# Kernel tuning notes

Measured on AMD Instinct MI355X. Metric: run time of the kernel, lower is better.

Reference implementation:

```python
import jax, jax.numpy as jnp
import numpy as np

DIM = 256
NUM_HEADS = 4
HEAD_DIM = DIM // NUM_HEADS
SCALE = HEAD_DIM ** -0.5
LN_EPS = 1e-5


def setup_inputs() -> dict:
    key = jax.random.key(0)
    ks = jax.random.split(key, 12)
    V, B, C, H, W = 3, 2, DIM, 32, 32
    s = 0.02
    return {
        "features": jax.random.normal(ks[0], (V, B, C, H, W), jnp.float32),
        "Wq": jax.random.normal(ks[1], (DIM, DIM), jnp.float32) * s,
        "bq": jnp.zeros((DIM,), jnp.float32),
        "Wk": jax.random.normal(ks[2], (DIM, DIM), jnp.float32) * s,
        "bk": jnp.zeros((DIM,), jnp.float32),
        "Wv": jax.random.normal(ks[3], (DIM, DIM), jnp.float32) * s,
        "bv": jnp.zeros((DIM,), jnp.float32),
        "Wp": jax.random.normal(ks[4], (DIM, DIM), jnp.float32) * s,
        "bp": jnp.zeros((DIM,), jnp.float32),
        "gamma": jnp.ones((DIM,), jnp.float32),
        "beta": jnp.zeros((DIM,), jnp.float32),
    }


def reference(features, Wq, bq, Wk, bk, Wv, bv, Wp, bp, gamma, beta):
    V, B, C, H, W = features.shape
    N = H * W
    L = V * N
    # concat views along token axis: [B, V*N, C]
    x = features.reshape(V, B, C, N).transpose(1, 0, 3, 2).reshape(B, L, C)
    # QKV projections (torch Linear: x @ W.T + b)
    q = (x @ Wq.T + bq).reshape(B, L, NUM_HEADS, HEAD_DIM).transpose(0, 2, 1, 3)
    k = (x @ Wk.T + bk).reshape(B, L, NUM_HEADS, HEAD_DIM).transpose(0, 2, 1, 3)
    v = (x @ Wv.T + bv).reshape(B, L, NUM_HEADS, HEAD_DIM).transpose(0, 2, 1, 3)
    # full attention (chunked loop in original is exact, dropout off in eval)
    attn = jax.nn.softmax(jnp.einsum('bhqd,bhkd->bhqk', q, k) * SCALE, axis=-1)
    o = jnp.einsum('bhqk,bhkd->bhqd', attn, v)  # [B, H, L, D]
    o = o.transpose(0, 2, 1, 3).reshape(B, L, C)
    # output proj + LayerNorm
    o = o @ Wp.T + bp
    mu = jnp.mean(o, axis=-1, keepdims=True)
    var = jnp.mean(jnp.square(o - mu), axis=-1, keepdims=True)
    o = (o - mu) * jax.lax.rsqrt(var + LN_EPS) * gamma + beta
    # mean over views, back to [B, C, H, W]
    o = o.reshape(B, V, N, C).mean(axis=1)
    return o.reshape(B, H, W, C).transpose(0, 3, 1, 2)
```

## Files before the change

### kernel.cpp

```cpp
#include <hip/hip_runtime.h>
#include <hip/hip_bf16.h>

#define V_ 3
#define B_ 2
#define C_ 256
#define N_ 1024
#define L_ 3072
#define NH 4
#define DH 64
#define SCALE 0.125f
#define LOG2E 1.44269504088896340736f

typedef __attribute__((ext_vector_type(8))) short short8;
typedef __attribute__((ext_vector_type(4))) float floatx4;
typedef unsigned short u16;
typedef unsigned int u32;

__device__ __forceinline__ u16 f2bf(float f) {
    union { float f; u32 u; } c; c.f = f;
    u32 u = c.u;
    u32 lsb = (u >> 16) & 1u;
    u += 0x7fffu + lsb;
    return (u16)(u >> 16);
}
__device__ __forceinline__ u32 pk_bf16(float a, float b) {
    __hip_bfloat162 h = __float22bfloat162_rn(make_float2(a, b));
    union { __hip_bfloat162 h; u32 u; } cv; cv.h = h; return cv.u;
}

__global__ __launch_bounds__(256) void k_prep_gather(
    const float* __restrict__ feat,
    const float* __restrict__ Wq, const float* __restrict__ Wk,
    const float* __restrict__ Wv, const float* __restrict__ Wp,
    u16* __restrict__ x, u16* __restrict__ Wb) {
    int bid = blockIdx.x;
    int t = threadIdx.x;
    if (bid < 384) {
        __shared__ u16 tile[64][66];
        int n0 = (bid & 15) << 6;
        int c0 = ((bid >> 4) & 3) << 6;
        int b  = (bid >> 6) & 1;
        int v  = bid >> 7;
        const float* src = feat + ((size_t)((v * B_ + b) * C_ + c0)) * N_ + n0;
        for (int i = 0; i < 8; ++i) {
            int idx = i * 256 + t;
            int cl = idx >> 5;
            int np2 = idx & 31;
            float2 f = *(const float2*)(src + (size_t)cl * N_ + np2 * 2);
            *(u32*)&tile[cl][np2 * 2] = pk_bf16(f.x, f.y);
        }
        __syncthreads();
        u16* dst = x + ((size_t)(b * L_ + v * N_ + n0)) * C_ + c0;
        for (int i = 0; i < 8; ++i) {
            int idx = i * 256 + t;
            int nl = idx >> 5;
            int cl = (idx & 31) * 2;
            u32 uu = (u32)tile[cl][nl] | ((u32)tile[cl + 1][nl] << 16);
            *(u32*)(dst + (size_t)nl * C_ + cl) = uu;
        }
    } else {
        int idx = (bid - 384) * 256 + t;
        int g0 = idx * 16;
        int m = g0 >> 16;
        const float* src = (m == 0) ? Wq : (m == 1) ? Wk : (m == 2) ? Wv : Wp;
        int off = g0 & 65535;
#pragma unroll
        for (int e = 0; e < 8; ++e) {
            float2 f = *(const float2*)(src + off + e * 2);
            ((u32*)(Wb + g0))[e] = pk_bf16(f.x, f.y);
        }
    }
}


__global__ __launch_bounds__(64) void k_qkv(
    const u16* __restrict__ x, const u16* __restrict__ Wb,
    const float* __restrict__ bq, const float* __restrict__ bk,
    const float* __restrict__ bv,
    u16* __restrict__ Qf, u16* __restrict__ Kf, u16* __restrict__ Vf) {
    int bid = blockIdx.x;
    int npc = bid & 3;
    int rest = bid >> 2;
    int m  = rest / 192;
    int rb = rest % 192;
    int b  = rb / 96;
    int r0 = (rb % 96) * 32;
    int lane = threadIdx.x;
    int quad = lane >> 4, m16 = lane & 15;

    const u16* xrow0 = x + ((size_t)(b * L_ + r0 + m16)) * C_ + quad * 8;
    const u16* xrow1 = xrow0 + (size_t)16 * C_;
    short8 a0[8], a1[8];
#pragma unroll
    for (int kc = 0; kc < 8; ++kc) {
        a0[kc] = *(const short8*)(xrow0 + kc * 32);
        a1[kc] = *(const short8*)(xrow1 + kc * 32);
    }

    const u16* W   = Wb + (size_t)m * 65536;
    const float* bs = (m == 0) ? bq : (m == 1) ? bk : bv;
    float scale = (m == 0) ? (SCALE * LOG2E) : 1.0f;

#pragma unroll
    for (int np = npc * 2; np < npc * 2 + 2; ++np) {
        int nt0 = np * 2;
        const u16* w0 = W + (size_t)(nt0 * 16 + m16) * C_ + quad * 8;
        const u16* w1 = w0 + 16 * C_;
        short8 wf0[8], wf1[8];
#pragma unroll
        for (int kc = 0; kc < 8; ++kc) {
            wf0[kc] = *(const short8*)(w0 + kc * 32);
            wf1[kc] = *(const short8*)(w1 + kc * 32);
        }
        floatx4 acc00 = {0.f,0.f,0.f,0.f}, acc01 = {0.f,0.f,0.f,0.f};
        floatx4 acc10 = {0.f,0.f,0.f,0.f}, acc11 = {0.f,0.f,0.f,0.f};
#pragma unroll
        for (int kc = 0; kc < 8; ++kc) {
            acc00 = __builtin_amdgcn_mfma_f32_16x16x32_bf16(a0[kc], wf0[kc], acc00, 0, 0, 0);
            acc01 = __builtin_amdgcn_mfma_f32_16x16x32_bf16(a0[kc], wf1[kc], acc01, 0, 0, 0);
            acc10 = __builtin_amdgcn_mfma_f32_16x16x32_bf16(a1[kc], wf0[kc], acc10, 0, 0, 0);
            acc11 = __builtin_amdgcn_mfma_f32_16x16x32_bf16(a1[kc], wf1[kc], acc11, 0, 0, 0);
        }
#pragma unroll
        for (int gi = 0; gi < 2; ++gi)
#pragma unroll
        for (int half = 0; half < 2; ++half) {
            int dout = (nt0 + half) * 16 + m16;
            float bias = bs[dout];
            int h = dout >> 6, dh = dout & 63;
            size_t bh = (size_t)(b * NH + h);
            floatx4 acc = gi ? (half ? acc11 : acc10) : (half ? acc01 : acc00);
            float f0 = (acc[0] + bias) * scale, f1 = (acc[1] + bias) * scale;
            float f2 = (acc[2] + bias) * scale, f3 = (acc[3] + bias) * scale;
            int lr0 = r0 + gi * 16 + quad * 4;
            if (m == 2) {
                int tile = lr0 >> 6, kk = lr0 & 63;
                int halfv = kk >> 5, quadp = (kk >> 3) & 3, j0 = kk & 7;
                int ntv = dh >> 4, m16pp = dh & 15;
                u32* p = (u32*)(Vf + (bh * 48 + tile) * 4096 +
                                ((size_t)((ntv * 2 + halfv) * 64 + quadp * 16 + m16pp)) * 8 + j0);
                p[0] = pk_bf16(f0, f1);
                p[1] = pk_bf16(f2, f3);
            } else {
                int cc = dh >> 5, quadp = (dh >> 3) & 3, j = dh & 7;
                u32 p01 = pk_bf16(f0, f1);
                u32 p23 = pk_bf16(f2, f3);
                if (m == 0) {
#pragma unroll
                    for (int r = 0; r < 4; ++r) {
                        int lr = lr0 + r;
                        int grp = lr >> 4, m16p = lr & 15;
                        u32 pk = (r < 2) ? p01 : p23;
                        u16 val = (r & 1) ? (u16)(pk >> 16) : (u16)pk;
                        Qf[(bh * 192 + grp) * 1024 +
                           (size_t)(cc * 64 + quadp * 16 + m16p) * 8 + j] = val;
                    }
                } else {
#pragma unroll
                    for (int r = 0; r < 4; ++r) {
                        int lr = lr0 + r;
                        int tile = lr >> 6, rr = lr & 63;
                        int ntk = rr >> 4, m16p = rr & 15;
                        u32 pk = (r < 2) ? p01 : p23;
                        u16 val = (r & 1) ? (u16)(pk >> 16) : (u16)pk;
                        Kf[(bh * 48 + tile) * 4096 +
                           (size_t)((ntk * 2 + cc) * 64 + quadp * 16 + m16p) * 8 + j] = val;
                    }
                }
            }
        }
    }
}

__global__ __launch_bounds__(256, 3) void k_attn(
    const u16* __restrict__ Qf, const u16* __restrict__ Kf,
    const u16* __restrict__ Vf, u16* __restrict__ o) {
    __shared__ __align__(16) u16 p_lds[4][32][72];
    __shared__ float o_red[3][32][65];
    __shared__ float l_red[3][32];
    int bid = blockIdx.x;
    int qt = bid % 96;
    int h  = (bid / 96) & 3;
    int b  = bid / 384;
    int lane = threadIdx.x & 63;
    int w    = threadIdx.x >> 6;
    int quad = lane >> 4, m16 = lane & 15;
    int q0 = qt * 32;
    size_t bh = (size_t)(b * NH + h);

    const u16* qbase = Qf + (bh * 192 + qt * 2) * 1024 + (size_t)lane * 8;
    const u16* kbase = Kf + bh * 48 * 4096 + (size_t)lane * 8;
    const u16* vbase = Vf + bh * 48 * 4096 + (size_t)lane * 8;

    short8 aq[2][2];
    aq[0][0] = *(const short8*)(qbase);
    aq[0][1] = *(const short8*)(qbase + 512);
    aq[1][0] = *(const short8*)(qbase + 1024);
    aq[1][1] = *(const short8*)(qbase + 1536);

    float l_s[2][4];
    floatx4 o_acc[2][4];
#pragma unroll
    for (int g = 0; g < 2; ++g)
#pragma unroll
        for (int r = 0; r < 4; ++r) {
            l_s[g][r] = 0.f;
            o_acc[g][r] = (floatx4){0.f, 0.f, 0.f, 0.f};
        }

    int kt0 = w * 12;
    short8 kb[8], vb[8];
#pragma unroll
    for (int f = 0; f < 8; ++f)
        kb[f] = *(const short8*)(kbase + (size_t)kt0 * 4096 + f * 512);

    for (int i = 0; i < 12; ++i) {
        size_t tbase = (size_t)(kt0 + i) * 4096;
#pragma unroll
        for (int f = 0; f < 8; ++f)
            vb[f] = *(const short8*)(vbase + tbase + f * 512);
        floatx4 s[2][4];
#pragma unroll
        for (int g = 0; g < 2; ++g)
#pragma unroll
            for (int nt = 0; nt < 4; ++nt) {
                floatx4 z = {0.f, 0.f, 0.f, 0.f};
                z = __builtin_amdgcn_mfma_f32_16x16x32_bf16(aq[g][0], kb[nt * 2], z, 0, 0, 0);
                s[g][nt] = __builtin_amdgcn_mfma_f32_16x16x32_bf16(aq[g][1], kb[nt * 2 + 1], z, 0, 0, 0);
            }
#pragma unroll
        for (int g = 0; g < 2; ++g) {
            int rb = g * 16 + quad * 4;
#pragma unroll
            for (int nt = 0; nt < 4; ++nt) {
                float p0 = __builtin_amdgcn_exp2f(s[g][nt][0]);
                float p1 = __builtin_amdgcn_exp2f(s[g][nt][1]);
                float p2 = __builtin_amdgcn_exp2f(s[g][nt][2]);
                float p3 = __builtin_amdgcn_exp2f(s[g][nt][3]);
                l_s[g][0] += p0; l_s[g][1] += p1;
                l_s[g][2] += p2; l_s[g][3] += p3;
                u32 q01 = pk_bf16(p0, p1);
                u32 q23 = pk_bf16(p2, p3);
                int col = nt * 16 + m16;
                p_lds[w][rb + 0][col] = (u16)q01;
                p_lds[w][rb + 1][col] = (u16)(q01 >> 16);
                p_lds[w][rb + 2][col] = (u16)q23;
                p_lds[w][rb + 3][col] = (u16)(q23 >> 16);
            }
        }
        if (i < 11) {
#pragma unroll
            for (int f = 0; f < 8; ++f)
                kb[f] = *(const short8*)(kbase + tbase + 4096 + f * 512);
        }
#pragma unroll
        for (int g = 0; g < 2; ++g) {
            short8 ap0 = *(const short8*)(&p_lds[w][g * 16 + m16][quad * 8]);
            short8 ap1 = *(const short8*)(&p_lds[w][g * 16 + m16][32 + quad * 8]);
#pragma unroll
            for (int nt = 0; nt < 4; ++nt) {
                o_acc[g][nt] = __builtin_amdgcn_mfma_f32_16x16x32_bf16(ap0, vb[nt * 2], o_acc[g][nt], 0, 0, 0);
                o_acc[g][nt] = __builtin_amdgcn_mfma_f32_16x16x32_bf16(ap1, vb[nt * 2 + 1], o_acc[g][nt], 0, 0, 0);
            }
        }
    }
    float l_row[2][4];
#pragma unroll
    for (int g = 0; g < 2; ++g)
#pragma unroll
        for (int r = 0; r < 4; ++r) {
            float ps = l_s[g][r];
            ps += __shfl_xor(ps, 1); ps += __shfl_xor(ps, 2);
            ps += __shfl_xor(ps, 4); ps += __shfl_xor(ps, 8);
            l_row[g][r] = ps;
        }
    if (w > 0) {
#pragma unroll
        for (int g = 0; g < 2; ++g) {
#pragma unroll
            for (int nt = 0; nt < 4; ++nt)
#pragma unroll
                for (int r = 0; r < 4; ++r)
                    o_red[w - 1][g * 16 + quad * 4 + r][nt * 16 + m16] = o_acc[g][nt][r];
            if (m16 == 0)
#pragma unroll
                for (int r = 0; r < 4; ++r)
                    l_red[w - 1][g * 16 + quad * 4 + r] = l_row[g][r];
        }
    }
    __syncthreads();
    if (w == 0) {
#pragma unroll
        for (int g = 0; g < 2; ++g) {
            float l_tot[4];
#pragma unroll
            for (int r = 0; r < 4; ++r) {
                int rw = g * 16 + quad * 4 + r;
                l_tot[r] = __builtin_amdgcn_rcpf(
                    l_row[g][r] + l_red[0][rw] + l_red[1][rw] + l_red[2][rw]);
            }
#pragma unroll
            for (int nt = 0; nt < 4; ++nt)
#pragma unroll
                for (int r = 0; r < 4; ++r) {
                    int rw = g * 16 + quad * 4 + r;
                    int col = nt * 16 + m16;
                    float tot = o_acc[g][nt][r] + o_red[0][rw][col] + o_red[1][rw][col] + o_red[2][rw][col];
                    o[((size_t)(b * L_ + q0 + rw)) * C_ + h * 64 + col] = f2bf(tot * l_tot[r]);
                }
        }
    }
}

__global__ __launch_bounds__(256) void k_proj_ln(
    const u16* __restrict__ o, const u16* __restrict__ Wpb,
    const float* __restrict__ bp,
    const float* __restrict__ gamma, const float* __restrict__ beta,
    float* __restrict__ out) {
    __shared__ float sred[4][16];
    __shared__ float sred2[4][16];
    __shared__ float tile[16][257];
    int bid = blockIdx.x;
    int b  = bid >> 6;
    int n0 = (bid & 63) << 4;
    int lane = threadIdx.x & 63;
    int w    = threadIdx.x >> 6;
    int quad = lane >> 4, m16 = lane & 15;

    float outacc[4][4];
#pragma unroll
    for (int j = 0; j < 4; ++j)
#pragma unroll
        for (int r = 0; r < 4; ++r) outacc[j][r] = 0.f;

    const u16* orow = o + ((size_t)(b * L_ + n0 + m16)) * C_ + quad * 8;
    short8 a[8];
#pragma unroll
    for (int kc = 0; kc < 8; ++kc) a[kc] = *(const short8*)(orow + kc * 32);

    for (int v = 0; v < V_; ++v) {
        float pr[4][4];
#pragma unroll
        for (int j = 0; j < 4; ++j) {
            int nt = w * 4 + j;
            const u16* wrow = Wpb + (size_t)(nt * 16 + m16) * C_ + quad * 8;
            floatx4 acc = {0.f, 0.f, 0.f, 0.f};
#pragma unroll
            for (int kc = 0; kc < 8; ++kc) {
                short8 bfr = *(const short8*)(wrow + kc * 32);
                acc = __builtin_amdgcn_mfma_f32_16x16x32_bf16(a[kc], bfr, acc, 0, 0, 0);
            }
            float bias = bp[nt * 16 + m16];
#pragma unroll
            for (int r = 0; r < 4; ++r) pr[j][r] = acc[r] + bias;
        }
        if (v < V_ - 1) {
            const u16* onext = o + ((size_t)(b * L_ + (v + 1) * N_ + n0 + m16)) * C_ + quad * 8;
#pragma unroll
            for (int kc = 0; kc < 8; ++kc) a[kc] = *(const short8*)(onext + kc * 32);
        }
#pragma unroll
        for (int r = 0; r < 4; ++r) {
            float sm = pr[0][r] + pr[1][r] + pr[2][r] + pr[3][r];
            sm += __shfl_xor(sm, 1); sm += __shfl_xor(sm, 2);
            sm += __shfl_xor(sm, 4); sm += __shfl_xor(sm, 8);
            if (m16 == 0) sred[w][quad * 4 + r] = sm;
        }
        __syncthreads();
        float mu[4];
#pragma unroll
        for (int r = 0; r < 4; ++r) {
            int row = quad * 4 + r;
            mu[r] = (sred[0][row] + sred[1][row] + sred[2][row] + sred[3][row]) * (1.0f / C_);
        }
#pragma unroll
        for (int r = 0; r < 4; ++r) {
            float sq = 0.f;
#pragma unroll
            for (int j = 0; j < 4; ++j) { float d = pr[j][r] - mu[r]; sq += d * d; }
            sq += __shfl_xor(sq, 1); sq += __shfl_xor(sq, 2);
            sq += __shfl_xor(sq, 4); sq += __shfl_xor(sq, 8);
            if (m16 == 0) sred2[w][quad * 4 + r] = sq;
        }
        __syncthreads();
        float rs[4];
#pragma unroll
        for (int r = 0; r < 4; ++r) {
            int row = quad * 4 + r;
            float var = (sred2[0][row] + sred2[1][row] + sred2[2][row] + sred2[3][row]) * (1.0f / C_);
            rs[r] = __builtin_amdgcn_rsqf(var + 1e-5f);
        }
#pragma unroll
        for (int j = 0; j < 4; ++j) {
            int c = (w * 4 + j) * 16 + m16;
            float g  = gamma[c];
            float be = beta[c];
#pragma unroll
            for (int r = 0; r < 4; ++r)
                outacc[j][r] += (pr[j][r] - mu[r]) * rs[r] * g + be;
        }
        __syncthreads();
    }
#pragma unroll
    for (int j = 0; j < 4; ++j) {
        int c = (w * 4 + j) * 16 + m16;
#pragma unroll
        for (int r = 0; r < 4; ++r)
            tile[quad * 4 + r][c] = outacc[j][r] * (1.0f / 3.0f);
    }
    __syncthreads();
    int c = threadIdx.x;
    float* op = out + ((size_t)(b * C_ + c)) * N_ + n0;
#pragma unroll
    for (int row = 0; row < 16; ++row)
        op[row] = tile[row][c];
}

extern "C" void kernel_launch(void* const* d_in, const int* in_sizes, int n_in,
                              void* d_out, int out_size, void* d_ws, size_t ws_size,
                              hipStream_t stream) {
    (void)in_sizes; (void)n_in; (void)out_size; (void)ws_size;
    const float* feat  = (const float*)d_in[0];
    const float* Wq    = (const float*)d_in[1];
    const float* bq    = (const float*)d_in[2];
    const float* Wk    = (const float*)d_in[3];
    const float* bk    = (const float*)d_in[4];
    const float* Wv    = (const float*)d_in[5];
    const float* bv    = (const float*)d_in[6];
    const float* Wp    = (const float*)d_in[7];
    const float* bp    = (const float*)d_in[8];
    const float* gamma = (const float*)d_in[9];
    const float* beta  = (const float*)d_in[10];
    float* out = (float*)d_out;

    size_t SZ = (size_t)B_ * L_ * C_;
    u16* x   = (u16*)d_ws;
    u16* Qf  = x + SZ;
    u16* Kf  = Qf + SZ;
    u16* Vf  = Kf + SZ;
    u16* o   = Vf + SZ;
    u16* Wb  = o + SZ;

    k_prep_gather<<<dim3(448), dim3(256), 0, stream>>>(feat, Wq, Wk, Wv, Wp, x, Wb);
    k_qkv<<<dim3(2304), dim3(64), 0, stream>>>(x, Wb, bq, bk, bv, Qf, Kf, Vf);
    k_attn<<<dim3(768), dim3(256), 0, stream>>>(Qf, Kf, Vf, o);
    k_proj_ln<<<dim3(128), dim3(256), 0, stream>>>(o, Wb + 3 * 65536, bp, gamma, beta, out);
}
```

Before: 137.4 us.

## Enlarge attention query tile, transpose MFMA operands, split proj-LN from view mean

The attention kernel now handles 48 query rows per block instead of 32, which cuts the grid from 768 to 512 blocks and reuses each K/V fragment across three query groups. It swaps MFMA operand order so P is written to LDS with vector stores and the cross-wave reduction shares LDS with the P buffer. Output stores become vectorized bf16 pairs. The projection+LayerNorm kernel now runs one view per block (384 blocks instead of 128) and writes a bf16 intermediate, and a new kernel averages the views and transposes to the output layout. This adds a launch and bf16 rounding before the mean, and the lower occupancy bound (2 blocks) may reduce latency hiding.

```diff
diff --git a/kernel.cpp b/kernel.cpp
--- a/kernel.cpp
+++ b/kernel.cpp
@@ -172,41 +172,40 @@
     }
 }
 
-__global__ __launch_bounds__(256, 3) void k_attn(
+__global__ __launch_bounds__(256, 2) void k_attn(
     const u16* __restrict__ Qf, const u16* __restrict__ Kf,
     const u16* __restrict__ Vf, u16* __restrict__ o) {
-    __shared__ __align__(16) u16 p_lds[4][32][72];
-    __shared__ float o_red[3][32][65];
-    __shared__ float l_red[3][32];
+    __shared__ __align__(16) char smem[36864];
+    __shared__ float l_red[3][3][16];
+    u16* PL = (u16*)smem;
+    float* o_red = (float*)smem;
     int bid = blockIdx.x;
-    int qt = bid % 96;
-    int h  = (bid / 96) & 3;
-    int b  = bid / 384;
+    int qt = bid & 63;
+    int h  = (bid >> 6) & 3;
+    int b  = bid >> 8;
     int lane = threadIdx.x & 63;
     int w    = threadIdx.x >> 6;
     int quad = lane >> 4, m16 = lane & 15;
-    int q0 = qt * 32;
+    int q0 = qt * 48;
     size_t bh = (size_t)(b * NH + h);
 
-    const u16* qbase = Qf + (bh * 192 + qt * 2) * 1024 + (size_t)lane * 8;
+    const u16* qbase = Qf + (bh * 192 + qt * 3) * 1024 + (size_t)lane * 8;
     const u16* kbase = Kf + bh * 48 * 4096 + (size_t)lane * 8;
     const u16* vbase = Vf + bh * 48 * 4096 + (size_t)lane * 8;
 
-    short8 aq[2][2];
-    aq[0][0] = *(const short8*)(qbase);
-    aq[0][1] = *(const short8*)(qbase + 512);
-    aq[1][0] = *(const short8*)(qbase + 1024);
-    aq[1][1] = *(const short8*)(qbase + 1536);
-
-    float l_s[2][4];
-    floatx4 o_acc[2][4];
-#pragma unroll
-    for (int g = 0; g < 2; ++g)
-#pragma unroll
-        for (int r = 0; r < 4; ++r) {
-            l_s[g][r] = 0.f;
-            o_acc[g][r] = (floatx4){0.f, 0.f, 0.f, 0.f};
-        }
+    short8 aq[3][2];
+#pragma unroll
+    for (int g = 0; g < 3; ++g) {
+        aq[g][0] = *(const short8*)(qbase + g * 1024);
+        aq[g][1] = *(const short8*)(qbase + g * 1024 + 512);
+    }
+
+    float l_s[3] = {0.f, 0.f, 0.f};
+    floatx4 o_acc[3][4];
+#pragma unroll
+    for (int g = 0; g < 3; ++g)
+#pragma unroll
+        for (int nt = 0; nt < 4; ++nt) o_acc[g][nt] = (floatx4){0.f, 0.f, 0.f, 0.f};
 
     int kt0 = w * 12;
     short8 kb[8], vb[8];
@@ -219,33 +218,34 @@
 #pragma unroll
         for (int f = 0; f < 8; ++f)
             vb[f] = *(const short8*)(vbase + tbase + f * 512);
-        floatx4 s[2][4];
-#pragma unroll
-        for (int g = 0; g < 2; ++g)
+#pragma unroll
+        for (int g = 0; g < 3; ++g) {
+            floatx4 s[4];
 #pragma unroll
             for (int nt = 0; nt < 4; ++nt) {
                 floatx4 z = {0.f, 0.f, 0.f, 0.f};
-                z = __builtin_amdgcn_mfma_f32_16x16x32_bf16(aq[g][0], kb[nt * 2], z, 0, 0, 0);
-                s[g][nt] = __builtin_amdgcn_mfma_f32_16x16x32_bf16(aq[g][1], kb[nt * 2 + 1], z, 0, 0, 0);
+                z = __builtin_amdgcn_mfma_f32_16x16x32_bf16(kb[nt * 2], aq[g][0], z, 0, 0, 0);
+                s[nt] = __builtin_amdgcn_mfma_f32_16x16x32_bf16(kb[nt * 2 + 1], aq[g][1], z, 0, 0, 0);
             }
-#pragma unroll
-        for (int g = 0; g < 2; ++g) {
-            int rb = g * 16 + quad * 4;
+            u16* plrow = PL + (((w * 3 + g) * 16) + m16) * 72;
+            float lsum = 0.f;
 #pragma unroll
             for (int nt = 0; nt < 4; ++nt) {
-                float p0 = __builtin_amdgcn_exp2f(s[g][nt][0]);
-                float p1 = __builtin_amdgcn_exp2f(s[g][nt][1]);
-                float p2 = __builtin_amdgcn_exp2f(s[g][nt][2]);
-                float p3 = __builtin_amdgcn_exp2f(s[g][nt][3]);
-                l_s[g][0] += p0; l_s[g][1] += p1;
-                l_s[g][2] += p2; l_s[g][3] += p3;
-                u32 q01 = pk_bf16(p0, p1);
-                u32 q23 = pk_bf16(p2, p3);
-                int col = nt * 16 + m16;
-                p_lds[w][rb + 0][col] = (u16)q01;
-                p_lds[w][rb + 1][col] = (u16)(q01 >> 16);
-                p_lds[w][rb + 2][col] = (u16)q23;
-                p_lds[w][rb + 3][col] = (u16)(q23 >> 16);
+                float p0 = __builtin_amdgcn_exp2f(s[nt][0]);
+                float p1 = __builtin_amdgcn_exp2f(s[nt][1]);
+                float p2 = __builtin_amdgcn_exp2f(s[nt][2]);
+                float p3 = __builtin_amdgcn_exp2f(s[nt][3]);
+                lsum += (p0 + p1) + (p2 + p3);
+                uint2 pk; pk.x = pk_bf16(p0, p1); pk.y = pk_bf16(p2, p3);
+                *(uint2*)(plrow + nt * 16 + quad * 4) = pk;
+            }
+            l_s[g] += lsum;
+            short8 bp0 = *(const short8*)(plrow + quad * 8);
+            short8 bp1 = *(const short8*)(plrow + 32 + quad * 8);
+#pragma unroll
+            for (int nt = 0; nt < 4; ++nt) {
+                o_acc[g][nt] = __builtin_amdgcn_mfma_f32_16x16x32_bf16(vb[nt * 2], bp0, o_acc[g][nt], 0, 0, 0);
+                o_acc[g][nt] = __builtin_amdgcn_mfma_f32_16x16x32_bf16(vb[nt * 2 + 1], bp1, o_acc[g][nt], 0, 0, 0);
             }
         }
         if (i < 11) {
@@ -253,61 +253,43 @@
             for (int f = 0; f < 8; ++f)
                 kb[f] = *(const short8*)(kbase + tbase + 4096 + f * 512);
         }
-#pragma unroll
-        for (int g = 0; g < 2; ++g) {
-            short8 ap0 = *(const short8*)(&p_lds[w][g * 16 + m16][quad * 8]);
-            short8 ap1 = *(const short8*)(&p_lds[w][g * 16 + m16][32 + quad * 8]);
-#pragma unroll
-            for (int nt = 0; nt < 4; ++nt) {
-                o_acc[g][nt] = __builtin_amdgcn_mfma_f32_16x16x32_bf16(ap0, vb[nt * 2], o_acc[g][nt], 0, 0, 0);
-                o_acc[g][nt] = __builtin_amdgcn_mfma_f32_16x16x32_bf16(ap1, vb[nt * 2 + 1], o_acc[g][nt], 0, 0, 0);
-            }
-        }
-    }
-    float l_row[2][4];
-#pragma unroll
-    for (int g = 0; g < 2; ++g)
-#pragma unroll
-        for (int r = 0; r < 4; ++r) {
-            float ps = l_s[g][r];
-            ps += __shfl_xor(ps, 1); ps += __shfl_xor(ps, 2);
-            ps += __shfl_xor(ps, 4); ps += __shfl_xor(ps, 8);
-            l_row[g][r] = ps;
-        }
+    }
+    float l_row[3];
+#pragma unroll
+    for (int g = 0; g < 3; ++g) {
+        float ps = l_s[g];
+        ps += __shfl_xor(ps, 16);
+        ps += __shfl_xor(ps, 32);
+        l_row[g] = ps;
+    }
+    __syncthreads();
     if (w > 0) {
 #pragma unroll
-        for (int g = 0; g < 2; ++g) {
+        for (int g = 0; g < 3; ++g) {
 #pragma unroll
             for (int nt = 0; nt < 4; ++nt)
-#pragma unroll
-                for (int r = 0; r < 4; ++r)
-                    o_red[w - 1][g * 16 + quad * 4 + r][nt * 16 + m16] = o_acc[g][nt][r];
-            if (m16 == 0)
-#pragma unroll
-                for (int r = 0; r < 4; ++r)
-                    l_red[w - 1][g * 16 + quad * 4 + r] = l_row[g][r];
+                *(floatx4*)&o_red[(((w - 1) * 3 + g) * 4 + nt) * 256 + lane * 4] = o_acc[g][nt];
+            if (quad == 0) l_red[w - 1][g][m16] = l_row[g];
         }
     }
     __syncthreads();
     if (w == 0) {
 #pragma unroll
-        for (int g = 0; g < 2; ++g) {
-            float l_tot[4];
-#pragma unroll
-            for (int r = 0; r < 4; ++r) {
-                int rw = g * 16 + quad * 4 + r;
-                l_tot[r] = __builtin_amdgcn_rcpf(
-                    l_row[g][r] + l_red[0][rw] + l_red[1][rw] + l_red[2][rw]);
+        for (int g = 0; g < 3; ++g) {
+            float lt = __builtin_amdgcn_rcpf(
+                l_row[g] + l_red[0][g][m16] + l_red[1][g][m16] + l_red[2][g][m16]);
+#pragma unroll
+            for (int nt = 0; nt < 4; ++nt) {
+                floatx4 tot = o_acc[g][nt];
+#pragma unroll
+                for (int w1 = 0; w1 < 3; ++w1)
+                    tot += *(const floatx4*)&o_red[((w1 * 3 + g) * 4 + nt) * 256 + lane * 4];
+                uint2 pk;
+                pk.x = pk_bf16(tot[0] * lt, tot[1] * lt);
+                pk.y = pk_bf16(tot[2] * lt, tot[3] * lt);
+                *(uint2*)(o + ((size_t)(b * L_ + q0 + g * 16 + m16)) * C_ +
+                          h * 64 + nt * 16 + quad * 4) = pk;
             }
-#pragma unroll
-            for (int nt = 0; nt < 4; ++nt)
-#pragma unroll
-                for (int r = 0; r < 4; ++r) {
-                    int rw = g * 16 + quad * 4 + r;
-                    int col = nt * 16 + m16;
-                    float tot = o_acc[g][nt][r] + o_red[0][rw][col] + o_red[1][rw][col] + o_red[2][rw][col];
-                    o[((size_t)(b * L_ + q0 + rw)) * C_ + h * 64 + col] = f2bf(tot * l_tot[r]);
-                }
         }
     }
 }
@@ -316,104 +298,110 @@
     const u16* __restrict__ o, const u16* __restrict__ Wpb,
     const float* __restrict__ bp,
     const float* __restrict__ gamma, const float* __restrict__ beta,
-    float* __restrict__ out) {
+    u16* __restrict__ oln) {
     __shared__ float sred[4][16];
     __shared__ float sred2[4][16];
-    __shared__ float tile[16][257];
     int bid = blockIdx.x;
-    int b  = bid >> 6;
     int n0 = (bid & 63) << 4;
+    int b  = (bid >> 6) & 1;
+    int v  = bid >> 7;
     int lane = threadIdx.x & 63;
     int w    = threadIdx.x >> 6;
     int quad = lane >> 4, m16 = lane & 15;
 
-    float outacc[4][4];
-#pragma unroll
-    for (int j = 0; j < 4; ++j)
-#pragma unroll
-        for (int r = 0; r < 4; ++r) outacc[j][r] = 0.f;
-
-    const u16* orow = o + ((size_t)(b * L_ + n0 + m16)) * C_ + quad * 8;
+    const u16* orow = o + ((size_t)(b * L_ + v * N_ + n0 + m16)) * C_ + quad * 8;
     short8 a[8];
 #pragma unroll
     for (int kc = 0; kc < 8; ++kc) a[kc] = *(const short8*)(orow + kc * 32);
 
-    for (int v = 0; v < V_; ++v) {
-        float pr[4][4];
-#pragma unroll
-        for (int j = 0; j < 4; ++j) {
-            int nt = w * 4 + j;
-            const u16* wrow = Wpb + (size_t)(nt * 16 + m16) * C_ + quad * 8;
-            floatx4 acc = {0.f, 0.f, 0.f, 0.f};
-#pragma unroll
-            for (int kc = 0; kc < 8; ++kc) {
-                short8 bfr = *(const short8*)(wrow + kc * 32);
-                acc = __builtin_amdgcn_mfma_f32_16x16x32_bf16(a[kc], bfr, acc, 0, 0, 0);
-            }
-            float bias = bp[nt * 16 + m16];
-#pragma unroll
-            for (int r = 0; r < 4; ++r) pr[j][r] = acc[r] + bias;
-        }
-        if (v < V_ - 1) {
-            const u16* onext = o + ((size_t)(b * L_ + (v + 1) * N_ + n0 + m16)) * C_ + quad * 8;
-#pragma unroll
-            for (int kc = 0; kc < 8; ++kc) a[kc] = *(const short8*)(onext + kc * 32);
-        }
-#pragma unroll
-        for (int r = 0; r < 4; ++r) {
-            float sm = pr[0][r] + pr[1][r] + pr[2][r] + pr[3][r];
-            sm += __shfl_xor(sm, 1); sm += __shfl_xor(sm, 2);
-            sm += __shfl_xor(sm, 4); sm += __shfl_xor(sm, 8);
-            if (m16 == 0) sred[w][quad * 4 + r] = sm;
-        }
-        __syncthreads();
-        float mu[4];
+    float pr[4][4];
+#pragma unroll
+    for (int j = 0; j < 4; ++j) {
+        int nt = w * 4 + j;
+        const u16* wrow = Wpb + (size_t)(nt * 16 + m16) * C_ + quad * 8;
+        floatx4 acc = {0.f, 0.f, 0.f, 0.f};
+#pragma unroll
+        for (int kc = 0; kc < 8; ++kc) {
+            short8 bfr = *(const short8*)(wrow + kc * 32);
+            acc = __builtin_amdgcn_mfma_f32_16x16x32_bf16(a[kc], bfr, acc, 0, 0, 0);
+        }
+        float bias = bp[nt * 16 + m16];
+#pragma unroll
+        for (int r = 0; r < 4; ++r) pr[j][r] = acc[r] + bias;
+    }
+#pragma unroll
+    for (int r = 0; r < 4; ++r) {
+        float sm = pr[0][r] + pr[1][r] + pr[2][r] + pr[3][r];
+        sm += __shfl_xor(sm, 1); sm += __shfl_xor(sm, 2);
+        sm += __shfl_xor(sm, 4); sm += __shfl_xor(sm, 8);
+        if (m16 == 0) sred[w][quad * 4 + r] = sm;
+    }
+    __syncthreads();
+    float mu[4];
+#pragma unroll
+    for (int r = 0; r < 4; ++r) {
+        int row = quad * 4 + r;
+        mu[r] = (sred[0][row] + sred[1][row] + sred[2][row] + sred[3][row]) * (1.0f / C_);
+    }
+#pragma unroll
+    for (int r = 0; r < 4; ++r) {
+        float sq = 0.f;
+#pragma unroll
+        for (int j = 0; j < 4; ++j) { float d = pr[j][r] - mu[r]; sq += d * d; }
+        sq += __shfl_xor(sq, 1); sq += __shfl_xor(sq, 2);
+        sq += __shfl_xor(sq, 4); sq += __shfl_xor(sq, 8);
+        if (m16 == 0) sred2[w][quad * 4 + r] = sq;
+    }
+    __syncthreads();
+    float rs[4];
+#pragma unroll
+    for (int r = 0; r < 4; ++r) {
+        int row = quad * 4 + r;
+        float var = (sred2[0][row] + sred2[1][row] + sred2[2][row] + sred2[3][row]) * (1.0f / C_);
+        rs[r] = __builtin_amdgcn_rsqf(var + 1e-5f);
+    }
+#pragma unroll
+    for (int j = 0; j < 4; ++j) {
+        int nt = w * 4 + j;
+        int c = nt * 16 + m16;
+        float g  = gamma[c];
+        float be = beta[c];
 #pragma unroll
         for (int r = 0; r < 4; ++r) {
             int row = quad * 4 + r;
-            mu[r] = (sred[0][row] + sred[1][row] + sred[2][row] + sred[3][row]) * (1.0f / C_);
-        }
-#pragma unroll
-        for (int r = 0; r < 4; ++r) {
-            float sq = 0.f;
-#pragma unroll
-            for (int j = 0; j < 4; ++j) { float d = pr[j][r] - mu[r]; sq += d * d; }
-            sq += __shfl_xor(sq, 1); sq += __shfl_xor(sq, 2);
-            sq += __shfl_xor(sq, 4); sq += __shfl_xor(sq, 8);
-            if (m16 == 0) sred2[w][quad * 4 + r] = sq;
-        }
-        __syncthreads();
-        float rs[4];
-#pragma unroll
-        for (int r = 0; r < 4; ++r) {
-            int row = quad * 4 + r;
-            float var = (sred2[0][row] + sred2[1][row] + sred2[2][row] + sred2[3][row]) * (1.0f / C_);
-            rs[r] = __builtin_amdgcn_rsqf(var + 1e-5f);
-        }
-#pragma unroll
-        for (int j = 0; j < 4; ++j) {
-            int c = (w * 4 + j) * 16 + m16;
-            float g  = gamma[c];
-            float be = beta[c];
-#pragma unroll
-            for (int r = 0; r < 4; ++r)
-                outacc[j][r] += (pr[j][r] - mu[r]) * rs[r] * g + be;
-        }
-        __syncthreads();
-    }
-#pragma unroll
-    for (int j = 0; j < 4; ++j) {
-        int c = (w * 4 + j) * 16 + m16;
-#pragma unroll
-        for (int r = 0; r < 4; ++r)
-            tile[quad * 4 + r][c] = outacc[j][r] * (1.0f / 3.0f);
+            oln[((size_t)((v * B_ + b) * N_ + n0 + row)) * C_ + c] =
+                f2bf((pr[j][r] - mu[r]) * rs[r] * g + be);
+        }
+    }
+}
+
+__global__ __launch_bounds__(256) void k_mean_t(
+    const u16* __restrict__ oln, float* __restrict__ out) {
+    __shared__ float tile[64][65];
+    int bid = blockIdx.x;
+    int n0 = (bid & 15) << 6;
+    int c0 = ((bid >> 4) & 3) << 6;
+    int b  = bid >> 6;
+    int t = threadIdx.x;
+    union { u32 u; float f; } cv;
+    for (int i = 0; i < 16; ++i) {
+        int idx = i * 256 + t;
+        int nl = idx >> 6, cl = idx & 63;
+        float sm = 0.f;
+#pragma unroll
+        for (int v = 0; v < 3; ++v) {
+            u16 raw = oln[((size_t)((v * B_ + b) * N_ + n0 + nl)) * C_ + c0 + cl];
+            cv.u = ((u32)raw) << 16;
+            sm += cv.f;
+        }
+        tile[cl][nl] = sm * (1.0f / 3.0f);
     }
     __syncthreads();
-    int c = threadIdx.x;
-    float* op = out + ((size_t)(b * C_ + c)) * N_ + n0;
-#pragma unroll
-    for (int row = 0; row < 16; ++row)
-        op[row] = tile[row][c];
+    for (int i = 0; i < 16; ++i) {
+        int idx = i * 256 + t;
+        int cl = idx >> 6, nl = idx & 63;
+        out[((size_t)(b * C_ + c0 + cl)) * N_ + n0 + nl] = tile[cl][nl];
+    }
 }
 
 extern "C" void kernel_launch(void* const* d_in, const int* in_sizes, int n_in,
@@ -440,9 +428,11 @@
     u16* Vf  = Kf + SZ;
     u16* o   = Vf + SZ;
     u16* Wb  = o + SZ;
+    u16* oln = Wb + 4 * 65536;
 
     k_prep_gather<<<dim3(448), dim3(256), 0, stream>>>(feat, Wq, Wk, Wv, Wp, x, Wb);
     k_qkv<<<dim3(2304), dim3(64), 0, stream>>>(x, Wb, bq, bk, bv, Qf, Kf, Vf);
-    k_attn<<<dim3(768), dim3(256), 0, stream>>>(Qf, Kf, Vf, o);
-    k_proj_ln<<<dim3(128), dim3(256), 0, stream>>>(o, Wb + 3 * 65536, bp, gamma, beta, out);
-}
+    k_attn<<<dim3(512), dim3(256), 0, stream>>>(Qf, Kf, Vf, o);
+    k_proj_ln<<<dim3(384), dim3(256), 0, stream>>>(o, Wb + 3 * 65536, bp, gamma, beta, oln);
+    k_mean_t<<<dim3(128), dim3(256), 0, stream>>>(oln, out);
+}
```

After: 134.3 us. 1.02x faster.
